# Optimization experiments

Hardware: AMD Instinct MI355X
Metric: run time of the kernel (lower is better)

Reference implementation:

```python
import jax, jax.numpy as jnp
import numpy as np

N_HEADS = 8
CHUNK = 512


def _mha(x, Wq, Wk, Wv, Wo, n_heads):
    # Standard no-bias multi-head self-attention; torch Linear => x @ W.T
    B, T, d = x.shape
    hd = d // n_heads
    q = (x @ Wq.T).reshape(B, T, n_heads, hd)
    k = (x @ Wk.T).reshape(B, T, n_heads, hd)
    v = (x @ Wv.T).reshape(B, T, n_heads, hd)
    scores = jnp.einsum('bqhd,bkhd->bhqk', q, k) / jnp.sqrt(jnp.asarray(hd, x.dtype))
    attn = jax.nn.softmax(scores, axis=-1)
    out = jnp.einsum('bhqk,bkhd->bqhd', attn, v).reshape(B, T, d)
    return out @ Wo.T


def _cross_chunk_attn(s, n_heads):
    # SDPA over chunk summaries with q=k=v=s (no projections inside)
    B, nc, d = s.shape
    hd = d // n_heads
    q = s.reshape(B, nc, n_heads, hd)
    scores = jnp.einsum('bqhd,bkhd->bhqk', q, q) / jnp.sqrt(jnp.asarray(hd, s.dtype))
    attn = jax.nn.softmax(scores, axis=-1)
    out = jnp.einsum('bhqk,bkhd->bqhd', attn, q).reshape(B, nc, d)
    return out


def setup_inputs() -> dict:
    key = jax.random.key(0)
    ks = jax.random.split(key, 6)
    B, T, d = 2, 16384, 512
    scale = 1.0 / np.sqrt(d)
    x = jax.random.normal(ks[0], (B, T, d), dtype=jnp.float32)
    Wq = jax.random.normal(ks[1], (d, d), dtype=jnp.float32) * scale
    Wk = jax.random.normal(ks[2], (d, d), dtype=jnp.float32) * scale
    Wv = jax.random.normal(ks[3], (d, d), dtype=jnp.float32) * scale
    Wo = jax.random.normal(ks[4], (d, d), dtype=jnp.float32) * scale
    Wg = jax.random.normal(ks[5], (d, d), dtype=jnp.float32) * scale
    return {'x': x, 'Wq': Wq, 'Wk': Wk, 'Wv': Wv, 'Wo': Wo, 'Wg': Wg}


def reference(x, Wq, Wk, Wv, Wo, Wg):
    B, T, d = x.shape
    pad = (CHUNK - T % CHUNK) % CHUNK
    if pad > 0:
        x = jnp.pad(x, ((0, 0), (0, pad), (0, 0)))
    T_padded = T + pad
    n_chunks = T_padded // CHUNK
    # 1) chunk: (B*n_chunks, CHUNK, d)
    chunked = x.reshape(B * n_chunks, CHUNK, d)
    # 2) local attention within each chunk
    local_out = _mha(chunked, Wq, Wk, Wv, Wo, N_HEADS)
    # 3) mean-pool summaries -> (B, n_chunks, d)
    summaries = local_out.mean(axis=1).reshape(B, n_chunks, d)
    # 4) global projection + cross-chunk SDPA
    global_ctx = _cross_chunk_attn(summaries @ Wg.T, N_HEADS)
    # 5) broadcast chunk context back to tokens
    enriched = local_out + global_ctx.reshape(B * n_chunks, 1, d)
    # 6) recombine and trim padding
    out = enriched.reshape(B, T_padded, d)
    if pad > 0:
        out = out[:, :T, :]
    return out
```

## Files before the change

kernel.cpp:

```cpp
#include <hip/hip_runtime.h>

typedef __attribute__((ext_vector_type(8))) short short8;
typedef __attribute__((ext_vector_type(4))) float f32x4;
typedef __attribute__((ext_vector_type(16))) float f32x16;

#define DEV static __device__ __forceinline__

DEV float bf2f(unsigned short u) {
  union { unsigned int u32; float f; } v; v.u32 = ((unsigned int)u) << 16; return v.f;
}
DEV unsigned short f2bf(float f) {
  union { float f; unsigned int u; } v; v.f = f;
  unsigned int r = v.u + 0x7fffu + ((v.u >> 16) & 1u);
  return (unsigned short)(r >> 16);
}
DEV unsigned cvtpk(float lo, float hi) {
  unsigned r;
  asm("v_cvt_pk_bf16_f32 %0, %1, %2" : "=v"(r) : "v"(lo), "v"(hi));
  return r;
}
DEV void plswap(unsigned &a, unsigned &b) {
  asm("v_permlane32_swap_b32 %0, %1" : "+v"(a), "+v"(b));
}
DEV short8 mk8(unsigned a, unsigned b, unsigned c, unsigned d) {
  union { unsigned u[4]; short8 v; } x;
  x.u[0] = a; x.u[1] = b; x.u[2] = c; x.u[3] = d; return x.v;
}
DEV float fexp2(float x) {
  float r;
  asm("v_exp_f32 %0, %1" : "=v"(r) : "v"(x));
  return r;
}

#define GLL16(g, l) __builtin_amdgcn_global_load_lds( \
    (const __attribute__((address_space(1))) void*)(g), \
    (__attribute__((address_space(3))) void*)(l), 16, 0, 0)

constexpr int D  = 512;
constexpr int BT = 32768;

__global__ __launch_bounds__(256) void k_convert(
    const float* __restrict__ x, const float* __restrict__ Wq, const float* __restrict__ Wk,
    const float* __restrict__ Wv, const float* __restrict__ Wo,
    unsigned short* __restrict__ xb, unsigned short* __restrict__ wqkv,
    unsigned short* __restrict__ wo_b) {
  int idx = blockIdx.x * 256 + threadIdx.x;
  const int NX4 = (BT * D) / 4;
  const float* src; unsigned short* dst; size_t i4;
  if (idx < NX4) {
    src = x; dst = xb; i4 = (size_t)idx * 4;
  } else {
    int t = idx - NX4;
    int w = t >> 16;
    int within = t & 65535;
    src = (w == 0) ? Wq : (w == 1) ? Wk : (w == 2) ? Wv : Wo;
    dst = (w < 3) ? (wqkv + (size_t)w * D * D) : wo_b;
    i4 = (size_t)within * 4;
  }
  float4 v = *(const float4*)(src + i4);
  ushort4 o; o.x = f2bf(v.x); o.y = f2bf(v.y); o.z = f2bf(v.z); o.w = f2bf(v.w);
  *(ushort4*)(dst + i4) = o;
}

template<int NBLK, int EPI>
__global__ __launch_bounds__(512, 4) void k_gemm(
    const unsigned short* __restrict__ A, const unsigned short* __restrict__ Bm,
    unsigned short* __restrict__ O0, unsigned short* __restrict__ O1,
    unsigned short* __restrict__ O2) {
  __shared__ unsigned short Ash[3][128 * 32];
  __shared__ unsigned short Bsh[3][256 * 32];
  const int tid = threadIdx.x;
  const int lane = tid & 63, w = tid >> 6;
  const int lr = lane & 15, lg = lane >> 4;
  const int cpx = gridDim.x >> 3;
  const int bid = blockIdx.x;
  const int work = (bid & 7) * cpx + (bid >> 3);
  const int nb = work % NBLK, mb = work / NBLK;
  const int m0 = mb * 128, n0 = nb * 256;
  const int wr = w >> 2, wc = w & 3;

  const int sr = lane >> 2;
  const int sg8 = ((lane & 3) ^ ((lane >> 3) & 3)) * 8;
  const unsigned short* gA  = A  + (size_t)(m0 + w * 16 + sr) * D + sg8;
  const unsigned short* gB0 = Bm + (size_t)(n0 + w * 16 + sr) * D + sg8;
  const unsigned short* gB1 = Bm + (size_t)(n0 + 128 + w * 16 + sr) * D + sg8;

  auto stage = [&](int kt, int b) {
    GLL16(gA  + kt * 32, &Ash[b][w * 512]);
    GLL16(gB0 + kt * 32, &Bsh[b][w * 512]);
    GLL16(gB1 + kt * 32, &Bsh[b][(128 + w * 16) * 32]);
  };

  f32x4 acc[4][4];
  #pragma unroll
  for (int m = 0; m < 4; ++m)
    #pragma unroll
    for (int n = 0; n < 4; ++n) acc[m][n] = (f32x4){0.f, 0.f, 0.f, 0.f};

  stage(0, 0);
  stage(1, 1);

  const int rdsw = (lg ^ ((lr >> 1) & 3)) * 8;

#define GSTEP(KT, WN) { \
    asm volatile("s_waitcnt vmcnt(" #WN ")" ::: "memory"); \
    __builtin_amdgcn_s_barrier(); \
    if ((KT) + 2 < 16) stage((KT) + 2, ((KT) + 2) % 3); \
    const unsigned short* Ac = Ash[(KT) % 3]; \
    const unsigned short* Bc = Bsh[(KT) % 3]; \
    short8 af[4], bf[4]; \
    _Pragma("unroll") \
    for (int m = 0; m < 4; ++m) \
      af[m] = *(const short8*)&Ac[(wr * 64 + m * 16 + lr) * 32 + rdsw]; \
    _Pragma("unroll") \
    for (int n = 0; n < 4; ++n) \
      bf[n] = *(const short8*)&Bc[(wc * 64 + n * 16 + lr) * 32 + rdsw]; \
    __builtin_amdgcn_s_setprio(1); \
    _Pragma("unroll") \
    for (int m = 0; m < 4; ++m) \
      _Pragma("unroll") \
      for (int n = 0; n < 4; ++n) \
        acc[m][n] = __builtin_amdgcn_mfma_f32_16x16x32_bf16(af[m], bf[n], acc[m][n], 0, 0, 0); \
    __builtin_amdgcn_s_setprio(0); \
  }

  GSTEP(0, 3)  GSTEP(1, 3)  GSTEP(2, 3)  GSTEP(3, 3)
  GSTEP(4, 3)  GSTEP(5, 3)  GSTEP(6, 3)  GSTEP(7, 3)
  GSTEP(8, 3)  GSTEP(9, 3)  GSTEP(10, 3) GSTEP(11, 3)
  GSTEP(12, 3) GSTEP(13, 3) GSTEP(14, 3) GSTEP(15, 0)
#undef GSTEP

  if (EPI == 1 && nb >= 4) {
    #pragma unroll
    for (int m = 0; m < 4; ++m) {
      #pragma unroll
      for (int n = 0; n < 4; ++n) {
        int e = (n0 - 1024) + wc * 64 + n * 16 + lr;
        int grow = m0 + wr * 64 + m * 16 + lg * 4;
        int bc = grow >> 9, key = grow & 511;
        ushort4 pk;
        pk.x = f2bf(acc[m][n][0]); pk.y = f2bf(acc[m][n][1]);
        pk.z = f2bf(acc[m][n][2]); pk.w = f2bf(acc[m][n][3]);
        *(ushort4*)&O2[(size_t)(bc * 512 + e) * 512 + key] = pk;
      }
    }
  } else {
    unsigned short* Od = O0;
    int cshift = 0;
    float cs = (EPI == 1 && nb < 2) ? 0.1803368801f : 1.0f;
    if (EPI == 1 && nb >= 2) { Od = O1; cshift = 512; }
    #pragma unroll
    for (int m = 0; m < 4; ++m) {
      #pragma unroll
      for (int n = 0; n < 4; ++n) {
        int col = n0 + wc * 64 + n * 16 + lr - cshift;
        #pragma unroll
        for (int r = 0; r < 4; ++r) {
          int row = m0 + wr * 64 + m * 16 + lg * 4 + r;
          Od[(size_t)row * D + col] = f2bf(acc[m][n][r] * cs);
        }
      }
    }
  }
}

__global__ __launch_bounds__(512, 4) void k_attn(
    const unsigned short* __restrict__ Q, const unsigned short* __restrict__ K,
    const unsigned short* __restrict__ Vt, unsigned short* __restrict__ attn_out) {
  __shared__ char lds[2][32768];
  const int tid = threadIdx.x;
  const int lane = tid & 63, w = tid >> 6;
  const int l31 = lane & 31, hl = lane >> 5;
  int work = ((blockIdx.x & 7) << 7) + (blockIdx.x >> 3);
  int qh = work & 1, h = (work >> 1) & 7, bc = work >> 4;
  int qbase = bc * 512 + qh * 256 + w * 32;

  short8 qf[4];
  {
    const unsigned short* qp = Q + (size_t)(qbase + l31) * D + h * 64 + hl * 8;
    #pragma unroll
    for (int ks = 0; ks < 4; ++ks) qf[ks] = *(const short8*)(qp + ks * 16);
  }

  const int lr3 = lane >> 3;
  const int srow = w * 8 + lr3;
  const int sq = (lane & 7) ^ ((lr3 + w) & 7);
  const unsigned short* gK = K  + (size_t)(bc * 512 + srow) * D + h * 64 + sq * 8;
  const unsigned short* gV = Vt + (size_t)(bc * 512 + h * 64 + srow) * D + sq * 8;
  auto STAGE = [&](int T, int B) {
    GLL16(gK + (size_t)(T * 128) * D,      &lds[B][w * 1024]);
    GLL16(gK + (size_t)(T * 128 + 64) * D, &lds[B][8192 + w * 1024]);
    GLL16(gV + T * 128,                    &lds[B][16384 + w * 1024]);
    GLL16(gV + T * 128 + 64,               &lds[B][24576 + w * 1024]);
  };

  f32x16 oA, oB;
  #pragma unroll
  for (int i = 0; i < 16; ++i) { oA[i] = 0.f; oB[i] = 0.f; }
  float mrun = -3e38f, lrun = 0.f;
  const int f0 = (l31 + (l31 >> 3)) & 7;
  const int f1 = (f0 + 4) & 7;

  STAGE(0, 0);

  #pragma unroll
  for (int t = 0; t < 4; ++t) {
    asm volatile("s_waitcnt vmcnt(0)" ::: "memory");
    __builtin_amdgcn_s_barrier();
    if (t < 3) STAGE(t + 1, (t + 1) & 1);
    #pragma unroll
    for (int s = 0; s < 2; ++s) {
      const char* kb = &lds[t & 1][s * 8192];
      const char* vb = &lds[t & 1][16384 + s * 8192];

      f32x16 sA, sB;
      #pragma unroll
      for (int i = 0; i < 16; ++i) { sA[i] = 0.f; sB[i] = 0.f; }
      __builtin_amdgcn_s_setprio(1);
      #pragma unroll
      for (int ks = 0; ks < 4; ++ks) {
        int c = ks * 2 + hl;
        short8 kf0 = *(const short8*)(kb + l31 * 128 + ((c ^ f0) << 4));
        short8 kf1 = *(const short8*)(kb + (32 + l31) * 128 + ((c ^ f1) << 4));
        sA = __builtin_amdgcn_mfma_f32_32x32x16_bf16(kf0, qf[ks], sA, 0, 0, 0);
        sB = __builtin_amdgcn_mfma_f32_32x32x16_bf16(kf1, qf[ks], sB, 0, 0, 0);
      }
      __builtin_amdgcn_s_setprio(0);

      float pm = fmaxf(sA[0], sA[1]);
      #pragma unroll
      for (int i = 2; i < 16; i += 2) pm = fmaxf(pm, fmaxf(sA[i], sA[i + 1]));
      #pragma unroll
      for (int i = 0; i < 16; i += 2) pm = fmaxf(pm, fmaxf(sB[i], sB[i + 1]));
      pm = fmaxf(pm, __shfl_xor(pm, 32));
      if (!__all(pm - mrun <= 8.f)) {
        float mnew = fmaxf(mrun, pm);
        float alpha = fexp2(mrun - mnew);
        mrun = mnew;
        lrun *= alpha;
        #pragma unroll
        for (int i = 0; i < 16; ++i) { oA[i] *= alpha; oB[i] *= alpha; }
      }
      float ls = 0.f;
      #pragma unroll
      for (int i = 0; i < 16; ++i) { float p = fexp2(sA[i] - mrun); sA[i] = p; ls += p; }
      #pragma unroll
      for (int i = 0; i < 16; ++i) { float p = fexp2(sB[i] - mrun); sB[i] = p; ls += p; }
      ls += __shfl_xor(ls, 32);
      lrun += ls;

      unsigned dA[8], dB[8];
      #pragma unroll
      for (int i = 0; i < 8; ++i) {
        dA[i] = cvtpk(sA[2 * i], sA[2 * i + 1]);
        dB[i] = cvtpk(sB[2 * i], sB[2 * i + 1]);
      }
      plswap(dA[0], dA[2]); plswap(dA[1], dA[3]);
      plswap(dA[4], dA[6]); plswap(dA[5], dA[7]);
      plswap(dB[0], dB[2]); plswap(dB[1], dB[3]);
      plswap(dB[4], dB[6]); plswap(dB[5], dB[7]);
      short8 pf[4] = { mk8(dA[0], dA[1], dA[2], dA[3]), mk8(dA[4], dA[5], dA[6], dA[7]),
                       mk8(dB[0], dB[1], dB[2], dB[3]), mk8(dB[4], dB[5], dB[6], dB[7]) };

      __builtin_amdgcn_s_setprio(1);
      #pragma unroll
      for (int k4 = 0; k4 < 4; ++k4) {
        int c = k4 * 2 + hl;
        short8 vf0 = *(const short8*)(vb + l31 * 128 + ((c ^ f0) << 4));
        short8 vf1 = *(const short8*)(vb + (32 + l31) * 128 + ((c ^ f1) << 4));
        oA = __builtin_amdgcn_mfma_f32_32x32x16_bf16(vf0, pf[k4], oA, 0, 0, 0);
        oB = __builtin_amdgcn_mfma_f32_32x32x16_bf16(vf1, pf[k4], oB, 0, 0, 0);
      }
      __builtin_amdgcn_s_setprio(0);
    }
  }

  __syncthreads();
  float inv = 1.f / lrun;
  const int x7 = l31 & 7;
  char* tr = &lds[0][0] + w * 4096;
  #pragma unroll
  for (int r = 0; r < 16; ++r) {
    int e0 = (r & 3) + 8 * (r >> 2) + 4 * hl;
    *(unsigned short*)(tr + ((l31 * 128 + e0 * 2) ^ (x7 << 4)))        = f2bf(oA[r] * inv);
    *(unsigned short*)(tr + ((l31 * 128 + (32 + e0) * 2) ^ (x7 << 4))) = f2bf(oB[r] * inv);
  }
  unsigned short* op = attn_out + (size_t)(qbase + l31) * D + h * 64 + hl * 32;
  #pragma unroll
  for (int s = 0; s < 4; ++s) {
    int slot = (hl * 4 + s) ^ x7;
    short8 v = *(const short8*)(tr + l31 * 128 + slot * 16);
    *(short8*)(op + s * 8) = v;
  }
}

__global__ __launch_bounds__(256) void k_mean(const unsigned short* __restrict__ lout,
                                              float* __restrict__ summ) {
  int bc = blockIdx.x;
  int col = blockIdx.y * 256 + threadIdx.x;
  const unsigned short* p = lout + (size_t)bc * 512 * 512 + col;
  float s = 0.f;
  #pragma unroll 8
  for (int r = 0; r < 512; ++r) s += bf2f(p[(size_t)r * 512]);
  summ[bc * 512 + col] = s * (1.f / 512.f);
}

__global__ __launch_bounds__(256) void k_sg(const float* __restrict__ summ,
                                            const float* __restrict__ Wg,
                                            float* __restrict__ sg) {
  __shared__ float srow[512];
  int m = blockIdx.x >> 1, half = blockIdx.x & 1;
  for (int i = threadIdx.x; i < 512; i += 256) srow[i] = summ[m * 512 + i];
  __syncthreads();
  int n = half * 256 + threadIdx.x;
  const float* wr = Wg + (size_t)n * 512;
  float s = 0.f;
  #pragma unroll 8
  for (int kk = 0; kk < 512; ++kk) s += srow[kk] * wr[kk];
  sg[m * 512 + n] = s;
}

__global__ __launch_bounds__(256) void k_gattn(const float* __restrict__ sg,
                                               float* __restrict__ gctx) {
  __shared__ float qs[32][64];
  __shared__ float sc[32][32];
  int b = blockIdx.x >> 3, h = blockIdx.x & 7;
  int tid = threadIdx.x;
  for (int i = tid; i < 2048; i += 256) {
    int r = i >> 6, e = i & 63;
    qs[r][e] = sg[(size_t)(b * 32 + r) * 512 + h * 64 + e];
  }
  __syncthreads();
  for (int p = tid; p < 1024; p += 256) {
    int qi = p >> 5, ki = p & 31;
    float s = 0.f;
    #pragma unroll 8
    for (int e = 0; e < 64; ++e) s += qs[qi][e] * qs[ki][e];
    sc[qi][ki] = s * 0.125f;
  }
  __syncthreads();
  if (tid < 32) {
    float mx = -1e30f;
    for (int k2 = 0; k2 < 32; ++k2) mx = fmaxf(mx, sc[tid][k2]);
    float sm = 0.f;
    for (int k2 = 0; k2 < 32; ++k2) { float p = __expf(sc[tid][k2] - mx); sc[tid][k2] = p; sm += p; }
    float iv = 1.f / sm;
    for (int k2 = 0; k2 < 32; ++k2) sc[tid][k2] *= iv;
  }
  __syncthreads();
  for (int i = tid; i < 2048; i += 256) {
    int r = i >> 6, e = i & 63;
    float o = 0.f;
    #pragma unroll 8
    for (int k2 = 0; k2 < 32; ++k2) o += sc[r][k2] * qs[k2][e];
    gctx[(size_t)(b * 32 + r) * 512 + h * 64 + e] = o;
  }
}

__global__ __launch_bounds__(256) void k_final(const unsigned short* __restrict__ lout,
                                               const float* __restrict__ gctx,
                                               float* __restrict__ out) {
  size_t idx = (size_t)blockIdx.x * 256 + threadIdx.x;
  size_t i = idx * 4;
  int c = (int)(i & 511);
  int bcg = (int)(i >> 18);
  ushort4 lv = *(const ushort4*)(lout + i);
  float4 g = *(const float4*)(gctx + (size_t)bcg * 512 + c);
  float4 o;
  o.x = bf2f(lv.x) + g.x;
  o.y = bf2f(lv.y) + g.y;
  o.z = bf2f(lv.z) + g.z;
  o.w = bf2f(lv.w) + g.w;
  *(float4*)(out + i) = o;
}

extern "C" void kernel_launch(void* const* d_in, const int* in_sizes, int n_in,
                              void* d_out, int out_size, void* d_ws, size_t ws_size,
                              hipStream_t stream) {
  const float* x  = (const float*)d_in[0];
  const float* Wq = (const float*)d_in[1];
  const float* Wk = (const float*)d_in[2];
  const float* Wv = (const float*)d_in[3];
  const float* Wo = (const float*)d_in[4];
  const float* Wg = (const float*)d_in[5];
  float* out = (float*)d_out;

  char* ws = (char*)d_ws;
  unsigned short* xb   = (unsigned short*)(ws);
  unsigned short* q    = (unsigned short*)(ws + 33554432);
  unsigned short* kb   = (unsigned short*)(ws + 67108864);
  unsigned short* vt   = (unsigned short*)(ws + 100663296);
  unsigned short* wqkv = (unsigned short*)(ws + 134217728);
  unsigned short* wo_b = (unsigned short*)(ws + 135790592);
  float* summ = (float*)(ws + 136314880);
  float* sgp  = (float*)(ws + 136445952);
  float* gctx = (float*)(ws + 136577024);
  unsigned short* attn_out = xb;
  unsigned short* local_bf = q;

  k_convert<<<17408, 256, 0, stream>>>(x, Wq, Wk, Wv, Wo, xb, wqkv, wo_b);
  k_gemm<6, 1><<<1536, 512, 0, stream>>>(xb, wqkv, q, kb, vt);
  k_attn<<<1024, 512, 0, stream>>>(q, kb, vt, attn_out);
  k_gemm<2, 0><<<512, 512, 0, stream>>>(attn_out, wo_b, local_bf, nullptr, nullptr);
  k_mean<<<dim3(64, 2), 256, 0, stream>>>(local_bf, summ);
  k_sg<<<128, 256, 0, stream>>>(summ, Wg, sgp);
  k_gattn<<<16, 256, 0, stream>>>(sgp, gctx);
  k_final<<<16384, 256, 0, stream>>>(local_bf, gctx, out);
}
```

Baseline: 232.9 us.

## Fuse global-context add into output GEMM and reorder mean before projection

Because mean-pooling is linear, the summaries are now computed by averaging the attention output first and then multiplying by Wo in a small matvec kernel. This removes the dependency on the output projection, so the O-projection GEMM can run last with an epilogue that adds gctx and writes fp32 output directly. That eliminates the bf16 local_out round trip and the separate k_final pass. In the attention kernel, the softmax row-sum is now accumulated by an extra MFMA against a ones vector instead of a scalar reduction and shuffle. This adds matrix work but removes VALU adds. Summaries now come from fp32 Wo rather than the bf16 GEMM output, which changes rounding slightly.

```diff
diff --git a/kernel.cpp b/kernel.cpp
--- a/kernel.cpp
+++ b/kernel.cpp
@@ -66,7 +66,8 @@
 __global__ __launch_bounds__(512, 4) void k_gemm(
     const unsigned short* __restrict__ A, const unsigned short* __restrict__ Bm,
     unsigned short* __restrict__ O0, unsigned short* __restrict__ O1,
-    unsigned short* __restrict__ O2) {
+    unsigned short* __restrict__ O2, float* __restrict__ Of,
+    const float* __restrict__ gctx) {
   __shared__ unsigned short Ash[3][128 * 32];
   __shared__ unsigned short Bsh[3][256 * 32];
   const int tid = threadIdx.x;
@@ -144,6 +145,21 @@
         *(ushort4*)&O2[(size_t)(bc * 512 + e) * 512 + key] = pk;
       }
     }
+  } else if (EPI == 2) {
+    const float* grow = gctx + (size_t)(m0 >> 9) * 512;
+    #pragma unroll
+    for (int m = 0; m < 4; ++m) {
+      #pragma unroll
+      for (int n = 0; n < 4; ++n) {
+        int col = n0 + wc * 64 + n * 16 + lr;
+        float g = grow[col];
+        #pragma unroll
+        for (int r = 0; r < 4; ++r) {
+          int row = m0 + wr * 64 + m * 16 + lg * 4 + r;
+          Of[(size_t)row * D + col] = acc[m][n][r] + g;
+        }
+      }
+    }
   } else {
     unsigned short* Od = O0;
     int cshift = 0;
@@ -194,10 +210,11 @@
     GLL16(gV + T * 128 + 64,               &lds[B][24576 + w * 1024]);
   };
 
-  f32x16 oA, oB;
+  f32x16 oA, oB, lsacc;
   #pragma unroll
-  for (int i = 0; i < 16; ++i) { oA[i] = 0.f; oB[i] = 0.f; }
-  float mrun = -3e38f, lrun = 0.f;
+  for (int i = 0; i < 16; ++i) { oA[i] = 0.f; oB[i] = 0.f; lsacc[i] = 0.f; }
+  float mrun = -3e38f;
+  const short8 ones8 = mk8(0x3F803F80u, 0x3F803F80u, 0x3F803F80u, 0x3F803F80u);
   const int f0 = (l31 + (l31 >> 3)) & 7;
   const int f1 = (f0 + 4) & 7;
 
@@ -237,17 +254,14 @@
         float mnew = fmaxf(mrun, pm);
         float alpha = fexp2(mrun - mnew);
         mrun = mnew;
-        lrun *= alpha;
+        lsacc[0] *= alpha;
         #pragma unroll
         for (int i = 0; i < 16; ++i) { oA[i] *= alpha; oB[i] *= alpha; }
       }
-      float ls = 0.f;
-      #pragma unroll
-      for (int i = 0; i < 16; ++i) { float p = fexp2(sA[i] - mrun); sA[i] = p; ls += p; }
-      #pragma unroll
-      for (int i = 0; i < 16; ++i) { float p = fexp2(sB[i] - mrun); sB[i] = p; ls += p; }
-      ls += __shfl_xor(ls, 32);
-      lrun += ls;
+      #pragma unroll
+      for (int i = 0; i < 16; ++i) sA[i] = fexp2(sA[i] - mrun);
+      #pragma unroll
+      for (int i = 0; i < 16; ++i) sB[i] = fexp2(sB[i] - mrun);
 
       unsigned dA[8], dB[8];
       #pragma unroll
@@ -270,13 +284,14 @@
         short8 vf1 = *(const short8*)(vb + (32 + l31) * 128 + ((c ^ f1) << 4));
         oA = __builtin_amdgcn_mfma_f32_32x32x16_bf16(vf0, pf[k4], oA, 0, 0, 0);
         oB = __builtin_amdgcn_mfma_f32_32x32x16_bf16(vf1, pf[k4], oB, 0, 0, 0);
+        lsacc = __builtin_amdgcn_mfma_f32_32x32x16_bf16(ones8, pf[k4], lsacc, 0, 0, 0);
       }
       __builtin_amdgcn_s_setprio(0);
     }
   }
 
   __syncthreads();
-  float inv = 1.f / lrun;
+  float inv = 1.f / lsacc[0];
   const int x7 = l31 & 7;
   char* tr = &lds[0][0] + w * 4096;
   #pragma unroll
@@ -294,30 +309,30 @@
   }
 }
 
-__global__ __launch_bounds__(256) void k_mean(const unsigned short* __restrict__ lout,
-                                              float* __restrict__ summ) {
+__global__ __launch_bounds__(256) void k_mean(const unsigned short* __restrict__ src,
+                                              float* __restrict__ msum) {
   int bc = blockIdx.x;
   int col = blockIdx.y * 256 + threadIdx.x;
-  const unsigned short* p = lout + (size_t)bc * 512 * 512 + col;
+  const unsigned short* p = src + (size_t)bc * 512 * 512 + col;
   float s = 0.f;
   #pragma unroll 8
   for (int r = 0; r < 512; ++r) s += bf2f(p[(size_t)r * 512]);
-  summ[bc * 512 + col] = s * (1.f / 512.f);
-}
-
-__global__ __launch_bounds__(256) void k_sg(const float* __restrict__ summ,
-                                            const float* __restrict__ Wg,
-                                            float* __restrict__ sg) {
+  msum[bc * 512 + col] = s * (1.f / 512.f);
+}
+
+__global__ __launch_bounds__(256) void k_sg(const float* __restrict__ in,
+                                            const float* __restrict__ Wt,
+                                            float* __restrict__ outv) {
   __shared__ float srow[512];
   int m = blockIdx.x >> 1, half = blockIdx.x & 1;
-  for (int i = threadIdx.x; i < 512; i += 256) srow[i] = summ[m * 512 + i];
+  for (int i = threadIdx.x; i < 512; i += 256) srow[i] = in[m * 512 + i];
   __syncthreads();
   int n = half * 256 + threadIdx.x;
-  const float* wr = Wg + (size_t)n * 512;
+  const float* wr = Wt + (size_t)n * 512;
   float s = 0.f;
   #pragma unroll 8
   for (int kk = 0; kk < 512; ++kk) s += srow[kk] * wr[kk];
-  sg[m * 512 + n] = s;
+  outv[m * 512 + n] = s;
 }
 
 __global__ __launch_bounds__(256) void k_gattn(const float* __restrict__ sg,
@@ -355,23 +370,6 @@
     for (int k2 = 0; k2 < 32; ++k2) o += sc[r][k2] * qs[k2][e];
     gctx[(size_t)(b * 32 + r) * 512 + h * 64 + e] = o;
   }
-}
-
-__global__ __launch_bounds__(256) void k_final(const unsigned short* __restrict__ lout,
-                                               const float* __restrict__ gctx,
-                                               float* __restrict__ out) {
-  size_t idx = (size_t)blockIdx.x * 256 + threadIdx.x;
-  size_t i = idx * 4;
-  int c = (int)(i & 511);
-  int bcg = (int)(i >> 18);
-  ushort4 lv = *(const ushort4*)(lout + i);
-  float4 g = *(const float4*)(gctx + (size_t)bcg * 512 + c);
-  float4 o;
-  o.x = bf2f(lv.x) + g.x;
-  o.y = bf2f(lv.y) + g.y;
-  o.z = bf2f(lv.z) + g.z;
-  o.w = bf2f(lv.w) + g.w;
-  *(float4*)(out + i) = o;
 }
 
 extern "C" void kernel_launch(void* const* d_in, const int* in_sizes, int n_in,
@@ -396,14 +394,14 @@
   float* sgp  = (float*)(ws + 136445952);
   float* gctx = (float*)(ws + 136577024);
   unsigned short* attn_out = xb;
-  unsigned short* local_bf = q;
+  float* msum = (float*)(ws + 33554432);
 
   k_convert<<<17408, 256, 0, stream>>>(x, Wq, Wk, Wv, Wo, xb, wqkv, wo_b);
-  k_gemm<6, 1><<<1536, 512, 0, stream>>>(xb, wqkv, q, kb, vt);
+  k_gemm<6, 1><<<1536, 512, 0, stream>>>(xb, wqkv, q, kb, vt, nullptr, nullptr);
   k_attn<<<1024, 512, 0, stream>>>(q, kb, vt, attn_out);
-  k_gemm<2, 0><<<512, 512, 0, stream>>>(attn_out, wo_b, local_bf, nullptr, nullptr);
-  k_mean<<<dim3(64, 2), 256, 0, stream>>>(local_bf, summ);
+  k_mean<<<dim3(64, 2), 256, 0, stream>>>(attn_out, msum);
+  k_sg<<<128, 256, 0, stream>>>(msum, Wo, summ);
   k_sg<<<128, 256, 0, stream>>>(summ, Wg, sgp);
   k_gattn<<<16, 256, 0, stream>>>(sgp, gctx);
-  k_final<<<16384, 256, 0, stream>>>(local_bf, gctx, out);
-}
+  k_gemm<2, 2><<<512, 512, 0, stream>>>(attn_out, wo_b, nullptr, nullptr, nullptr, out, gctx);
+}
```

New measurement: 244.9 us. +5.1%, slower.

## Shrink attention blocks to 4 waves with 64-key tiles and 8 stages

Applied to the files above, without the earlier changes.

Splits each chunk/head attention job over four 128-query blocks of 4 waves instead of two 256-query blocks of 8 waves. K/V staging tiles shrink from 128 to 64 keys, which halves LDS per block and doubles the number of pipeline steps. The aim is more resident blocks and finer scheduling across CUs. The cost is that each block now reloads the same K/V tiles, so K/V global traffic per query doubles, and there are more barriers per key.

```diff
diff --git a/kernel.cpp b/kernel.cpp
--- a/kernel.cpp
+++ b/kernel.cpp
@@ -164,16 +164,16 @@
   }
 }
 
-__global__ __launch_bounds__(512, 4) void k_attn(
+__global__ __launch_bounds__(256, 5) void k_attn(
     const unsigned short* __restrict__ Q, const unsigned short* __restrict__ K,
     const unsigned short* __restrict__ Vt, unsigned short* __restrict__ attn_out) {
-  __shared__ char lds[2][32768];
+  __shared__ char lds[2][16384];
   const int tid = threadIdx.x;
   const int lane = tid & 63, w = tid >> 6;
   const int l31 = lane & 31, hl = lane >> 5;
-  int work = ((blockIdx.x & 7) << 7) + (blockIdx.x >> 3);
-  int qh = work & 1, h = (work >> 1) & 7, bc = work >> 4;
-  int qbase = bc * 512 + qh * 256 + w * 32;
+  int work = ((blockIdx.x & 7) << 8) + (blockIdx.x >> 3);
+  int qq = work & 3, h = (work >> 2) & 7, bc = work >> 5;
+  int qbase = bc * 512 + qq * 128 + w * 32;
 
   short8 qf[4];
   {
@@ -183,15 +183,18 @@
   }
 
   const int lr3 = lane >> 3;
-  const int srow = w * 8 + lr3;
-  const int sq = (lane & 7) ^ ((lr3 + w) & 7);
-  const unsigned short* gK = K  + (size_t)(bc * 512 + srow) * D + h * 64 + sq * 8;
-  const unsigned short* gV = Vt + (size_t)(bc * 512 + h * 64 + srow) * D + sq * 8;
+  const int sq0 = (lane & 7) ^ ((lr3 + w) & 7);
+  const int sq1 = sq0 ^ 4;
+  const int sr0 = w * 8 + lr3;
+  const unsigned short* gK0 = K  + (size_t)(bc * 512 + sr0) * D + h * 64 + sq0 * 8;
+  const unsigned short* gK1 = K  + (size_t)(bc * 512 + 32 + sr0) * D + h * 64 + sq1 * 8;
+  const unsigned short* gV0 = Vt + (size_t)(bc * 512 + h * 64 + sr0) * D + sq0 * 8;
+  const unsigned short* gV1 = Vt + (size_t)(bc * 512 + h * 64 + 32 + sr0) * D + sq1 * 8;
   auto STAGE = [&](int T, int B) {
-    GLL16(gK + (size_t)(T * 128) * D,      &lds[B][w * 1024]);
-    GLL16(gK + (size_t)(T * 128 + 64) * D, &lds[B][8192 + w * 1024]);
-    GLL16(gV + T * 128,                    &lds[B][16384 + w * 1024]);
-    GLL16(gV + T * 128 + 64,               &lds[B][24576 + w * 1024]);
+    GLL16(gK0 + (size_t)(T * 64) * D, &lds[B][w * 1024]);
+    GLL16(gK1 + (size_t)(T * 64) * D, &lds[B][4096 + w * 1024]);
+    GLL16(gV0 + T * 64,               &lds[B][8192 + w * 1024]);
+    GLL16(gV1 + T * 64,               &lds[B][12288 + w * 1024]);
   };
 
   f32x16 oA, oB;
@@ -199,80 +202,77 @@
   for (int i = 0; i < 16; ++i) { oA[i] = 0.f; oB[i] = 0.f; }
   float mrun = -3e38f, lrun = 0.f;
   const int f0 = (l31 + (l31 >> 3)) & 7;
-  const int f1 = (f0 + 4) & 7;
+  const int f1 = f0 ^ 4;
 
   STAGE(0, 0);
 
   #pragma unroll
-  for (int t = 0; t < 4; ++t) {
+  for (int t = 0; t < 8; ++t) {
     asm volatile("s_waitcnt vmcnt(0)" ::: "memory");
     __builtin_amdgcn_s_barrier();
-    if (t < 3) STAGE(t + 1, (t + 1) & 1);
-    #pragma unroll
-    for (int s = 0; s < 2; ++s) {
-      const char* kb = &lds[t & 1][s * 8192];
-      const char* vb = &lds[t & 1][16384 + s * 8192];
-
-      f32x16 sA, sB;
+    if (t < 7) STAGE(t + 1, (t + 1) & 1);
+    const char* kb = &lds[t & 1][0];
+    const char* vb = &lds[t & 1][8192];
+
+    f32x16 sA, sB;
+    #pragma unroll
+    for (int i = 0; i < 16; ++i) { sA[i] = 0.f; sB[i] = 0.f; }
+    __builtin_amdgcn_s_setprio(1);
+    #pragma unroll
+    for (int ks = 0; ks < 4; ++ks) {
+      int c = ks * 2 + hl;
+      short8 kf0 = *(const short8*)(kb + l31 * 128 + ((c ^ f0) << 4));
+      short8 kf1 = *(const short8*)(kb + (32 + l31) * 128 + ((c ^ f1) << 4));
+      sA = __builtin_amdgcn_mfma_f32_32x32x16_bf16(kf0, qf[ks], sA, 0, 0, 0);
+      sB = __builtin_amdgcn_mfma_f32_32x32x16_bf16(kf1, qf[ks], sB, 0, 0, 0);
+    }
+    __builtin_amdgcn_s_setprio(0);
+
+    float pm = fmaxf(sA[0], sA[1]);
+    #pragma unroll
+    for (int i = 2; i < 16; i += 2) pm = fmaxf(pm, fmaxf(sA[i], sA[i + 1]));
+    #pragma unroll
+    for (int i = 0; i < 16; i += 2) pm = fmaxf(pm, fmaxf(sB[i], sB[i + 1]));
+    pm = fmaxf(pm, __shfl_xor(pm, 32));
+    if (!__all(pm - mrun <= 8.f)) {
+      float mnew = fmaxf(mrun, pm);
+      float alpha = fexp2(mrun - mnew);
+      mrun = mnew;
+      lrun *= alpha;
       #pragma unroll
-      for (int i = 0; i < 16; ++i) { sA[i] = 0.f; sB[i] = 0.f; }
-      __builtin_amdgcn_s_setprio(1);
-      #pragma unroll
-      for (int ks = 0; ks < 4; ++ks) {
-        int c = ks * 2 + hl;
-        short8 kf0 = *(const short8*)(kb + l31 * 128 + ((c ^ f0) << 4));
-        short8 kf1 = *(const short8*)(kb + (32 + l31) * 128 + ((c ^ f1) << 4));
-        sA = __builtin_amdgcn_mfma_f32_32x32x16_bf16(kf0, qf[ks], sA, 0, 0, 0);
-        sB = __builtin_amdgcn_mfma_f32_32x32x16_bf16(kf1, qf[ks], sB, 0, 0, 0);
-      }
-      __builtin_amdgcn_s_setprio(0);
-
-      float pm = fmaxf(sA[0], sA[1]);
-      #pragma unroll
-      for (int i = 2; i < 16; i += 2) pm = fmaxf(pm, fmaxf(sA[i], sA[i + 1]));
-      #pragma unroll
-      for (int i = 0; i < 16; i += 2) pm = fmaxf(pm, fmaxf(sB[i], sB[i + 1]));
-      pm = fmaxf(pm, __shfl_xor(pm, 32));
-      if (!__all(pm - mrun <= 8.f)) {
-        float mnew = fmaxf(mrun, pm);
-        float alpha = fexp2(mrun - mnew);
-        mrun = mnew;
-        lrun *= alpha;
-        #pragma unroll
-        for (int i = 0; i < 16; ++i) { oA[i] *= alpha; oB[i] *= alpha; }
-      }
-      float ls = 0.f;
-      #pragma unroll
-      for (int i = 0; i < 16; ++i) { float p = fexp2(sA[i] - mrun); sA[i] = p; ls += p; }
-      #pragma unroll
-      for (int i = 0; i < 16; ++i) { float p = fexp2(sB[i] - mrun); sB[i] = p; ls += p; }
-      ls += __shfl_xor(ls, 32);
-      lrun += ls;
-
-      unsigned dA[8], dB[8];
-      #pragma unroll
-      for (int i = 0; i < 8; ++i) {
-        dA[i] = cvtpk(sA[2 * i], sA[2 * i + 1]);
-        dB[i] = cvtpk(sB[2 * i], sB[2 * i + 1]);
-      }
-      plswap(dA[0], dA[2]); plswap(dA[1], dA[3]);
-      plswap(dA[4], dA[6]); plswap(dA[5], dA[7]);
-      plswap(dB[0], dB[2]); plswap(dB[1], dB[3]);
-      plswap(dB[4], dB[6]); plswap(dB[5], dB[7]);
-      short8 pf[4] = { mk8(dA[0], dA[1], dA[2], dA[3]), mk8(dA[4], dA[5], dA[6], dA[7]),
-                       mk8(dB[0], dB[1], dB[2], dB[3]), mk8(dB[4], dB[5], dB[6], dB[7]) };
-
-      __builtin_amdgcn_s_setprio(1);
-      #pragma unroll
-      for (int k4 = 0; k4 < 4; ++k4) {
-        int c = k4 * 2 + hl;
-        short8 vf0 = *(const short8*)(vb + l31 * 128 + ((c ^ f0) << 4));
-        short8 vf1 = *(const short8*)(vb + (32 + l31) * 128 + ((c ^ f1) << 4));
-        oA = __builtin_amdgcn_mfma_f32_32x32x16_bf16(vf0, pf[k4], oA, 0, 0, 0);
-        oB = __builtin_amdgcn_mfma_f32_32x32x16_bf16(vf1, pf[k4], oB, 0, 0, 0);
-      }
-      __builtin_amdgcn_s_setprio(0);
-    }
+      for (int i = 0; i < 16; ++i) { oA[i] *= alpha; oB[i] *= alpha; }
+    }
+    float ls = 0.f;
+    #pragma unroll
+    for (int i = 0; i < 16; ++i) { float p = fexp2(sA[i] - mrun); sA[i] = p; ls += p; }
+    #pragma unroll
+    for (int i = 0; i < 16; ++i) { float p = fexp2(sB[i] - mrun); sB[i] = p; ls += p; }
+    ls += __shfl_xor(ls, 32);
+    lrun += ls;
+
+    unsigned dA[8], dB[8];
+    #pragma unroll
+    for (int i = 0; i < 8; ++i) {
+      dA[i] = cvtpk(sA[2 * i], sA[2 * i + 1]);
+      dB[i] = cvtpk(sB[2 * i], sB[2 * i + 1]);
+    }
+    plswap(dA[0], dA[2]); plswap(dA[1], dA[3]);
+    plswap(dA[4], dA[6]); plswap(dA[5], dA[7]);
+    plswap(dB[0], dB[2]); plswap(dB[1], dB[3]);
+    plswap(dB[4], dB[6]); plswap(dB[5], dB[7]);
+    short8 pf[4] = { mk8(dA[0], dA[1], dA[2], dA[3]), mk8(dA[4], dA[5], dA[6], dA[7]),
+                     mk8(dB[0], dB[1], dB[2], dB[3]), mk8(dB[4], dB[5], dB[6], dB[7]) };
+
+    __builtin_amdgcn_s_setprio(1);
+    #pragma unroll
+    for (int k4 = 0; k4 < 4; ++k4) {
+      int c = k4 * 2 + hl;
+      short8 vf0 = *(const short8*)(vb + l31 * 128 + ((c ^ f0) << 4));
+      short8 vf1 = *(const short8*)(vb + (32 + l31) * 128 + ((c ^ f1) << 4));
+      oA = __builtin_amdgcn_mfma_f32_32x32x16_bf16(vf0, pf[k4], oA, 0, 0, 0);
+      oB = __builtin_amdgcn_mfma_f32_32x32x16_bf16(vf1, pf[k4], oB, 0, 0, 0);
+    }
+    __builtin_amdgcn_s_setprio(0);
   }
 
   __syncthreads();
@@ -400,7 +400,7 @@
 
   k_convert<<<17408, 256, 0, stream>>>(x, Wq, Wk, Wv, Wo, xb, wqkv, wo_b);
   k_gemm<6, 1><<<1536, 512, 0, stream>>>(xb, wqkv, q, kb, vt);
-  k_attn<<<1024, 512, 0, stream>>>(q, kb, vt, attn_out);
+  k_attn<<<2048, 256, 0, stream>>>(q, kb, vt, attn_out);
   k_gemm<2, 0><<<512, 512, 0, stream>>>(attn_out, wo_b, local_bf, nullptr, nullptr);
   k_mean<<<dim3(64, 2), 256, 0, stream>>>(local_bf, summ);
   k_sg<<<128, 256, 0, stream>>>(summ, Wg, sgp);
```

Result: slower. 264.6 us (+13.6%).
